# Kernel tuning notes

Measured on AMD Instinct MI355X. Metric: run time of the kernel, lower is better.

## Reference

```python
import jax, jax.numpy as jnp
import numpy as np

N = 50000          # num nodes
E = 800000         # num edges (avg degree 16)
IN_C, HID_C, OUT_C = 128, 128, 64
LPA_ITER = 5


def setup_inputs() -> dict:
    key = jax.random.key(0)
    ks = jax.random.split(key, 8)
    x = jax.random.normal(ks[0], (N, IN_C), dtype=jnp.float32)
    soft_labels = jax.random.uniform(ks[1], (N, OUT_C), dtype=jnp.float32)
    edge_index = jax.random.randint(ks[2], (2, E), 0, N, dtype=jnp.int64)
    # learnable edge weights: abs() in the original, so keep them positive
    edge_attr = jax.random.uniform(ks[3], (E,), dtype=jnp.float32, minval=0.1, maxval=1.0)
    # GCNConv params (lin weight + bias)
    w1 = jax.random.normal(ks[4], (IN_C, HID_C), dtype=jnp.float32) / np.sqrt(IN_C)
    b1 = jnp.zeros((HID_C,), dtype=jnp.float32)
    w2 = jax.random.normal(ks[5], (HID_C, OUT_C), dtype=jnp.float32) / np.sqrt(HID_C)
    b2 = jnp.zeros((OUT_C,), dtype=jnp.float32)
    return {"x": x, "soft_labels": soft_labels, "edge_attr": edge_attr,
            "w1": w1, "b1": b1, "w2": w2, "b2": b2, "edge_index": edge_index}


def reference(x, soft_labels, edge_attr, w1, b1, w2, b2, edge_index):
    row, col = edge_index[0], edge_index[1]
    n = x.shape[0]
    # row-normalize the weighted sparse adjacency: A_n = D^{-1} A
    deg = jax.ops.segment_sum(edge_attr, row, num_segments=n)  # [N]
    deg_inv = jnp.where(deg == 0, 0.0, 1.0 / deg)              # inf -> 0
    val = deg_inv[row] * edge_attr                              # [E]

    def spmm(v):  # A_n @ v,  v: [N, F]
        return jax.ops.segment_sum(val[:, None] * v[col], row, num_segments=n)

    # eval mode: dropout(p=0.5, training=False) is identity
    h = jax.nn.relu(spmm(x @ w1) + b1)        # GCNConv 1 (normalize=False)
    logits = spmm(h @ w2) + b2                # GCNConv 2
    x_out = jax.nn.sigmoid(logits)

    labels = soft_labels
    for _ in range(LPA_ITER):                 # label propagation
        labels = spmm(labels)
    labels = jax.nn.sigmoid(labels)
    return (x_out, labels)
```

## Files before the change

### kernel.cpp

```cpp
#include <hip/hip_runtime.h>
#include <cstdint>
#include <cstddef>


#define WS_ALIGN(x) (((x) + 255) & ~((size_t)255))

typedef __attribute__((ext_vector_type(8))) short short8;
typedef __attribute__((ext_vector_type(4))) float floatx4;

__device__ __forceinline__ unsigned short f2bf(float f) {
    unsigned u = __float_as_uint(f);
    u += 0x7fffu + ((u >> 16) & 1u);
    return (unsigned short)(u >> 16);
}
__device__ __forceinline__ float bf2f(unsigned short h) {
    return __uint_as_float(((unsigned)h) << 16);
}
__device__ __forceinline__ float sigmoidf(float x) {
    return 1.f / (1.f + __expf(-x));
}

static const int NBLK = 256;
#define MAXNB 256

__launch_bounds__(256)
__global__ void binA_count(const int* __restrict__ row, int* __restrict__ bucket_count,
                           int* __restrict__ bases, int E, int chunk, int NB)
{
    __shared__ int hist[MAXNB];
    const int t = threadIdx.x;
    const int blk = blockIdx.x;
    if (t < NB) hist[t] = 0;
    __syncthreads();
    const int s = blk * chunk;
    const int e = min(E, s + chunk);
    for (int i = s + t; i < e; i += 256)
        atomicAdd(&hist[row[i] >> 8], 1);
    __syncthreads();
    if (t < NB)
        bases[blk * NB + t] = atomicAdd(&bucket_count[t], hist[t]);
}

__launch_bounds__(256)
__global__ void bin_scan(const int* __restrict__ bucket_count, int* __restrict__ bucket_start,
                         int NB)
{
    __shared__ int s[256];
    const int t = threadIdx.x;
    int v = (t < NB) ? bucket_count[t] : 0;
    s[t] = v;
    __syncthreads();
    for (int off = 1; off < 256; off <<= 1) {
        int u = (t >= off) ? s[t - off] : 0;
        __syncthreads();
        s[t] += u;
        __syncthreads();
    }
    int excl = s[t] - v;
    if (t <= NB) bucket_start[t] = excl;
}

__launch_bounds__(256)
__global__ void binA_scatter(const int* __restrict__ row, const int* __restrict__ colv,
                             const float* __restrict__ ea,
                             const int* __restrict__ bucket_start, const int* __restrict__ bases,
                             int2* __restrict__ bk, int E, int chunk, int NB)
{
    __shared__ int cur[MAXNB];
    const int t = threadIdx.x;
    const int blk = blockIdx.x;
    if (t < NB) cur[t] = bucket_start[t] + bases[blk * NB + t];
    __syncthreads();
    const int s = blk * chunk;
    const int e = min(E, s + chunk);
    for (int i = s + t; i < e; i += 256) {
        int r = row[i];
        int bin = r >> 8;
        int pos = atomicAdd(&cur[bin], 1);
        bk[pos] = make_int2(((r & 255) << 16) | colv[i], __float_as_int(ea[i]));
    }
}

__launch_bounds__(256)
__global__ void binB(const int2* __restrict__ bk, const int* __restrict__ bucket_start,
                     int* __restrict__ rowptr, int2* __restrict__ edges, int N)
{
    __shared__ int cnt[256];
    __shared__ float deg[256];
    __shared__ float inv[256];
    __shared__ int excl_s[256];
    __shared__ int cur[256];
    __shared__ int scantmp[256];
    const int b = blockIdx.x;
    const int t = threadIdx.x;
    const int s = bucket_start[b];
    const int e = bucket_start[b + 1];
    cnt[t] = 0;
    deg[t] = 0.f;
    __syncthreads();
    for (int i = s + t; i < e; i += 256) {
        int2 v = bk[i];
        int rl = ((unsigned)v.x) >> 16;
        atomicAdd(&cnt[rl], 1);
        atomicAdd(&deg[rl], __int_as_float(v.y));
    }
    __syncthreads();
    const int myc = cnt[t];
    scantmp[t] = myc;
    __syncthreads();
    for (int off = 1; off < 256; off <<= 1) {
        int u = (t >= off) ? scantmp[t - off] : 0;
        __syncthreads();
        scantmp[t] += u;
        __syncthreads();
    }
    const int excl = scantmp[t] - myc;
    excl_s[t] = excl;
    float d = deg[t];
    inv[t] = (d > 0.f) ? 1.f / d : 0.f;
    cur[t] = 0;
    const int gr = b * 256 + t;
    if (gr <= N) rowptr[gr] = s + excl;
    __syncthreads();
    for (int i = s + t; i < e; i += 256) {
        int2 v = bk[i];
        int rl = ((unsigned)v.x) >> 16;
        int c = v.x & 0xffff;
        int p = s + excl_s[rl] + atomicAdd(&cur[rl], 1);
        edges[p] = make_int2(c, __float_as_int(__int_as_float(v.y) * inv[rl]));
    }
}

__global__ void f32_to_bf16_kernel(const float* __restrict__ in, unsigned short* __restrict__ out,
                                   int n2)
{
    int i = blockIdx.x * 256 + threadIdx.x;
    if (i < n2) {
        float2 v = ((const float2*)in)[i];
        unsigned p = (unsigned)f2bf(v.x) | ((unsigned)f2bf(v.y) << 16);
        ((unsigned*)out)[i] = p;
    }
}

template<int COLS>
__global__ void pack_w_kernel(const float* __restrict__ W, unsigned short* __restrict__ Wp)
{
    const int total = (COLS / 16) * 4 * 64;
    int idx = blockIdx.x * 256 + threadIdx.x;
    if (idx >= total) return;
    const int l = idx & 63;
    const int t = (idx >> 6) & 3;
    const int ct = idx >> 8;
    const int kbase = t * 32 + (l >> 4) * 8;
    const int col = ct * 16 + (l & 15);
    unsigned short v[8];
#pragma unroll
    for (int j = 0; j < 8; ++j)
        v[j] = f2bf(W[(size_t)(kbase + j) * COLS + col]);
    uint4 o;
    o.x = (unsigned)v[0] | ((unsigned)v[1] << 16);
    o.y = (unsigned)v[2] | ((unsigned)v[3] << 16);
    o.z = (unsigned)v[4] | ((unsigned)v[5] << 16);
    o.w = (unsigned)v[6] | ((unsigned)v[7] << 16);
    *(uint4*)(Wp + (size_t)idx * 8) = o;
}

template<int COLS>
__launch_bounds__(256)
__global__ void gemm_mfma_f32a(const float* __restrict__ A,
                               const unsigned short* __restrict__ Wp,
                               unsigned short* __restrict__ C, int M)
{
    const int wave = threadIdx.x >> 6;
    const int lane = threadIdx.x & 63;
    const int row0 = blockIdx.x * 64 + wave * 16;
    const int m = lane & 15;
    const int q = lane >> 4;

    const int arow = row0 + m;
    const bool avalid = arow < M;
    short8 a[4];
#pragma unroll
    for (int t = 0; t < 4; ++t) {
        if (avalid) {
            float4 f0 = *(const float4*)(A + (size_t)arow * 128 + t * 32 + q * 8);
            float4 f1 = *(const float4*)(A + (size_t)arow * 128 + t * 32 + q * 8 + 4);
            a[t][0] = (short)f2bf(f0.x); a[t][1] = (short)f2bf(f0.y);
            a[t][2] = (short)f2bf(f0.z); a[t][3] = (short)f2bf(f0.w);
            a[t][4] = (short)f2bf(f1.x); a[t][5] = (short)f2bf(f1.y);
            a[t][6] = (short)f2bf(f1.z); a[t][7] = (short)f2bf(f1.w);
        } else {
            a[t] = (short8)0;
        }
    }

#pragma unroll
    for (int ct = 0; ct < COLS / 16; ++ct) {
        floatx4 acc = {0.f, 0.f, 0.f, 0.f};
#pragma unroll
        for (int t = 0; t < 4; ++t) {
            short8 b = *(const short8*)(Wp + (size_t)((ct * 4 + t) * 64 + lane) * 8);
            acc = __builtin_amdgcn_mfma_f32_16x16x32_bf16(a[t], b, acc, 0, 0, 0);
        }
        const int col = ct * 16 + m;
#pragma unroll
        for (int r = 0; r < 4; ++r) {
            int orow = row0 + q * 4 + r;
            if (orow < M)
                C[(size_t)orow * COLS + col] = f2bf(acc[r]);
        }
    }
}

template<int COLS>
__launch_bounds__(256)
__global__ void gemm_mfma(const unsigned short* __restrict__ A,
                          const unsigned short* __restrict__ Wp,
                          unsigned short* __restrict__ C, int M)
{
    const int wave = threadIdx.x >> 6;
    const int lane = threadIdx.x & 63;
    const int row0 = blockIdx.x * 64 + wave * 16;
    const int m = lane & 15;
    const int q = lane >> 4;

    const int arow = row0 + m;
    const bool avalid = arow < M;
    short8 a[4];
#pragma unroll
    for (int t = 0; t < 4; ++t) {
        if (avalid)
            a[t] = *(const short8*)(A + (size_t)arow * 128 + t * 32 + q * 8);
        else
            a[t] = (short8)0;
    }

#pragma unroll
    for (int ct = 0; ct < COLS / 16; ++ct) {
        floatx4 acc = {0.f, 0.f, 0.f, 0.f};
#pragma unroll
        for (int t = 0; t < 4; ++t) {
            short8 b = *(const short8*)(Wp + (size_t)((ct * 4 + t) * 64 + lane) * 8);
            acc = __builtin_amdgcn_mfma_f32_16x16x32_bf16(a[t], b, acc, 0, 0, 0);
        }
        const int col = ct * 16 + m;
#pragma unroll
        for (int r = 0; r < 4; ++r) {
            int orow = row0 + q * 4 + r;
            if (orow < M)
                C[(size_t)orow * COLS + col] = f2bf(acc[r]);
        }
    }
}

__launch_bounds__(256)
__global__ void spmm_f128_f64(const int* __restrict__ rowptr, const int2* __restrict__ edges,
                              const unsigned* __restrict__ srcA,
                              const unsigned short* __restrict__ srcB,
                              const float* __restrict__ bias,
                              unsigned* __restrict__ outA,
                              unsigned short* __restrict__ outB,
                              int n)
{
    const int row = blockIdx.x * 4 + (threadIdx.x >> 6);
    const int lane = threadIdx.x & 63;
    if (row >= n) return;
    const int s = rowptr[row];
    const int e = rowptr[row + 1];

    float ax[8], ay[8], ab[8];
#pragma unroll
    for (int j = 0; j < 8; ++j) { ax[j] = 0.f; ay[j] = 0.f; ab[j] = 0.f; }
    int i = s;
    for (; i + 8 <= e; i += 8) {
        int2 ed[8];
        unsigned ua[8];
        unsigned short ub[8];
#pragma unroll
        for (int j = 0; j < 8; ++j) ed[j] = edges[i + j];
#pragma unroll
        for (int j = 0; j < 8; ++j) ua[j] = srcA[(size_t)ed[j].x * 64 + lane];
#pragma unroll
        for (int j = 0; j < 8; ++j) ub[j] = srcB[(size_t)ed[j].x * 64 + lane];
#pragma unroll
        for (int j = 0; j < 8; ++j) {
            float w = __int_as_float(ed[j].y);
            ax[j] = fmaf(w, __uint_as_float(ua[j] << 16), ax[j]);
            ay[j] = fmaf(w, __uint_as_float(ua[j] & 0xffff0000u), ay[j]);
            ab[j] = fmaf(w, bf2f(ub[j]), ab[j]);
        }
    }
    for (; i < e; ++i) {
        int2 e0 = edges[i];
        unsigned ua = srcA[(size_t)e0.x * 64 + lane];
        unsigned short ub = srcB[(size_t)e0.x * 64 + lane];
        float w = __int_as_float(e0.y);
        ax[0] = fmaf(w, __uint_as_float(ua << 16), ax[0]);
        ay[0] = fmaf(w, __uint_as_float(ua & 0xffff0000u), ay[0]);
        ab[0] = fmaf(w, bf2f(ub), ab[0]);
    }
    float vx = ((ax[0] + ax[1]) + (ax[2] + ax[3])) + ((ax[4] + ax[5]) + (ax[6] + ax[7]));
    float vy = ((ay[0] + ay[1]) + (ay[2] + ay[3])) + ((ay[4] + ay[5]) + (ay[6] + ay[7]));
    float vb = ((ab[0] + ab[1]) + (ab[2] + ab[3])) + ((ab[4] + ab[5]) + (ab[6] + ab[7]));
    float2 b = *(const float2*)(bias + lane * 2);
    vx = fmaxf(vx + b.x, 0.f);
    vy = fmaxf(vy + b.y, 0.f);
    outA[(size_t)row * 64 + lane] = (unsigned)f2bf(vx) | ((unsigned)f2bf(vy) << 16);
    outB[(size_t)row * 64 + lane] = f2bf(vb);
}

__launch_bounds__(256)
__global__ void spmm_f64_f64(const int* __restrict__ rowptr, const int2* __restrict__ edges,
                             const unsigned short* __restrict__ srcA,
                             const unsigned short* __restrict__ srcB,
                             const float* __restrict__ bias,
                             float* __restrict__ outA,
                             unsigned short* __restrict__ outB,
                             int n)
{
    const int row = blockIdx.x * 4 + (threadIdx.x >> 6);
    const int lane = threadIdx.x & 63;
    if (row >= n) return;
    const int s = rowptr[row];
    const int e = rowptr[row + 1];

    float aa[8], ab[8];
#pragma unroll
    for (int j = 0; j < 8; ++j) { aa[j] = 0.f; ab[j] = 0.f; }
    int i = s;
    for (; i + 8 <= e; i += 8) {
        int2 ed[8];
        unsigned short ua[8], ub[8];
#pragma unroll
        for (int j = 0; j < 8; ++j) ed[j] = edges[i + j];
#pragma unroll
        for (int j = 0; j < 8; ++j) ua[j] = srcA[(size_t)ed[j].x * 64 + lane];
#pragma unroll
        for (int j = 0; j < 8; ++j) ub[j] = srcB[(size_t)ed[j].x * 64 + lane];
#pragma unroll
        for (int j = 0; j < 8; ++j) {
            float w = __int_as_float(ed[j].y);
            aa[j] = fmaf(w, bf2f(ua[j]), aa[j]);
            ab[j] = fmaf(w, bf2f(ub[j]), ab[j]);
        }
    }
    for (; i < e; ++i) {
        int2 e0 = edges[i];
        float w = __int_as_float(e0.y);
        aa[0] = fmaf(w, bf2f(srcA[(size_t)e0.x * 64 + lane]), aa[0]);
        ab[0] = fmaf(w, bf2f(srcB[(size_t)e0.x * 64 + lane]), ab[0]);
    }
    float va = ((aa[0] + aa[1]) + (aa[2] + aa[3])) + ((aa[4] + aa[5]) + (aa[6] + aa[7]));
    float vb = ((ab[0] + ab[1]) + (ab[2] + ab[3])) + ((ab[4] + ab[5]) + (ab[6] + ab[7]));
    outA[(size_t)row * 64 + lane] = sigmoidf(va + bias[lane]);
    outB[(size_t)row * 64 + lane] = f2bf(vb);
}

template<int ACT, bool OUT_BF16>
__launch_bounds__(256)
__global__ void spmm64_kernel(const int* __restrict__ rowptr, const int2* __restrict__ edges,
                              const unsigned short* __restrict__ src,
                              void* __restrict__ out, int n)
{
    const int row = blockIdx.x * 4 + (threadIdx.x >> 6);
    const int lane = threadIdx.x & 63;
    if (row >= n) return;
    const int s = rowptr[row];
    const int e = rowptr[row + 1];

    float a[8];
#pragma unroll
    for (int j = 0; j < 8; ++j) a[j] = 0.f;
    int i = s;
    for (; i + 8 <= e; i += 8) {
        int2 ed[8];
        float sv[8];
#pragma unroll
        for (int j = 0; j < 8; ++j) ed[j] = edges[i + j];
#pragma unroll
        for (int j = 0; j < 8; ++j) sv[j] = bf2f(src[(size_t)ed[j].x * 64 + lane]);
#pragma unroll
        for (int j = 0; j < 8; ++j) a[j] = fmaf(__int_as_float(ed[j].y), sv[j], a[j]);
    }
    for (; i < e; ++i) {
        int2 e0 = edges[i];
        a[0] = fmaf(__int_as_float(e0.y), bf2f(src[(size_t)e0.x * 64 + lane]), a[0]);
    }
    float v = ((a[0] + a[1]) + (a[2] + a[3])) + ((a[4] + a[5]) + (a[6] + a[7]));
    if (ACT == 3) v = sigmoidf(v);
    if (OUT_BF16)
        ((unsigned short*)out)[(size_t)row * 64 + lane] = f2bf(v);
    else
        ((float*)out)[(size_t)row * 64 + lane] = v;
}

extern "C" void kernel_launch(void* const* d_in, const int* in_sizes, int n_in,
                              void* d_out, int out_size, void* d_ws, size_t ws_size,
                              hipStream_t stream)
{
    const float* x    = (const float*)d_in[0];
    const float* soft = (const float*)d_in[1];
    const float* ea   = (const float*)d_in[2];
    const float* w1   = (const float*)d_in[3];
    const float* b1   = (const float*)d_in[4];
    const float* w2   = (const float*)d_in[5];
    const float* b2   = (const float*)d_in[6];
    const int*   eidx = (const int*)d_in[7];

    const int N = in_sizes[0] / 128;
    const int E = in_sizes[2];
    const int* row  = eidx;
    const int* colv = eidx + E;
    const int NB = (N + 255) / 256;
    const int chunk = (E + NBLK - 1) / NBLK;

    uint8_t* ws = (uint8_t*)d_ws;
    size_t off = 0;
    auto alloc = [&](size_t bytes) -> void* {
        void* p = ws + off;
        off += WS_ALIGN(bytes);
        return p;
    };
    int*  bucket_count = (int*) alloc((size_t)NB * 4);
    int*  bucket_start = (int*) alloc(((size_t)NB + 1) * 4);
    int*  bases        = (int*) alloc((size_t)NBLK * NB * 4);
    int*  rowptr       = (int*) alloc(((size_t)N + 1) * 4);
    int2* bk           = (int2*)alloc((size_t)E * 8);
    int2* edges        = (int2*)alloc((size_t)E * 8);
    unsigned short* w1p     = (unsigned short*)alloc((size_t)128 * 128 * 2);
    unsigned short* w2p     = (unsigned short*)alloc((size_t)128 * 64 * 2);
    unsigned short* xw1b    = (unsigned short*)alloc((size_t)N * 128 * 2);
    unsigned short* hb      = (unsigned short*)alloc((size_t)N * 128 * 2);
    unsigned short* logitsb = (unsigned short*)alloc((size_t)N * 64 * 2);
    unsigned short* softb   = (unsigned short*)alloc((size_t)N * 64 * 2);
    unsigned short* labA    = (unsigned short*)alloc((size_t)N * 64 * 2);
    unsigned short* labB    = (unsigned short*)alloc((size_t)N * 64 * 2);

    float* out0 = (float*)d_out;
    float* out1 = out0 + (size_t)N * 64;

    hipMemsetAsync(bucket_count, 0, (size_t)NB * 4, stream);

    binA_count<<<NBLK, 256, 0, stream>>>(row, bucket_count, bases, E, chunk, NB);
    bin_scan<<<1, 256, 0, stream>>>(bucket_count, bucket_start, NB);
    binA_scatter<<<NBLK, 256, 0, stream>>>(row, colv, ea, bucket_start, bases, bk, E, chunk, NB);
    binB<<<NB, 256, 0, stream>>>(bk, bucket_start, rowptr, edges, N);

    const int ns2 = (N * 64) / 2;
    f32_to_bf16_kernel<<<(ns2 + 255) / 256, 256, 0, stream>>>(soft, softb, ns2);
    pack_w_kernel<128><<<8, 256, 0, stream>>>(w1, w1p);
    pack_w_kernel<64><<<4, 256, 0, stream>>>(w2, w2p);

    const int gGemm = (N + 63) / 64;
    const int gSp   = (N + 3) / 4;

    gemm_mfma_f32a<128><<<gGemm, 256, 0, stream>>>(x, w1p, xw1b, N);

    spmm_f128_f64<<<gSp, 256, 0, stream>>>(rowptr, edges, (const unsigned*)xw1b, softb,
                                           b1, (unsigned*)hb, labA, N);

    gemm_mfma<64><<<gGemm, 256, 0, stream>>>(hb, w2p, logitsb, N);

    spmm_f64_f64<<<gSp, 256, 0, stream>>>(rowptr, edges, logitsb, labA, b2, out0, labB, N);

    spmm64_kernel<0, true ><<<gSp, 256, 0, stream>>>(rowptr, edges, labB, labA, N);
    spmm64_kernel<0, true ><<<gSp, 256, 0, stream>>>(rowptr, edges, labA, labB, N);
    spmm64_kernel<3, false><<<gSp, 256, 0, stream>>>(rowptr, edges, labB, out1, N);
}
```

Measured before the change: 361.9 us.

## Split wavefront into two half-waves gathering wider vectors per edge in SpMM kernels

Each 64-lane wavefront now processes two edges at once, with each 32-lane half loading wider packed bf16 vectors (uint2 or unsigned) per feature slice. The halves are combined with a cross-lane shuffle before the write. Edge records are read with nontemporal loads. The aim is fewer, wider gather transactions per row and fewer serial edge iterations. The cost is an extra shuffle reduction and idle half-waves on odd tail edges.

```diff
diff --git a/kernel.cpp b/kernel.cpp
--- a/kernel.cpp
+++ b/kernel.cpp
@@ -13,11 +13,23 @@
     u += 0x7fffu + ((u >> 16) & 1u);
     return (unsigned short)(u >> 16);
 }
+__device__ __forceinline__ float bf_lo(unsigned u) { return __uint_as_float(u << 16); }
+__device__ __forceinline__ float bf_hi(unsigned u) { return __uint_as_float(u & 0xffff0000u); }
 __device__ __forceinline__ float bf2f(unsigned short h) {
     return __uint_as_float(((unsigned)h) << 16);
 }
+__device__ __forceinline__ unsigned pack_bf2(float a, float b) {
+    return (unsigned)f2bf(a) | ((unsigned)f2bf(b) << 16);
+}
 __device__ __forceinline__ float sigmoidf(float x) {
     return 1.f / (1.f + __expf(-x));
+}
+__device__ __forceinline__ int2 ld_nt_int2(const int2* p) {
+    long long v = __builtin_nontemporal_load((const long long*)p);
+    int2 r;
+    r.x = (int)(unsigned)(v & 0xffffffffLL);
+    r.y = (int)(v >> 32);
+    return r;
 }
 
 static const int NBLK = 256;
@@ -137,8 +149,7 @@
     int i = blockIdx.x * 256 + threadIdx.x;
     if (i < n2) {
         float2 v = ((const float2*)in)[i];
-        unsigned p = (unsigned)f2bf(v.x) | ((unsigned)f2bf(v.y) << 16);
-        ((unsigned*)out)[i] = p;
+        ((unsigned*)out)[i] = pack_bf2(v.x, v.y);
     }
 }
 
@@ -254,144 +265,228 @@
 }
 
 __launch_bounds__(256)
-__global__ void spmm_f128_f64(const int* __restrict__ rowptr, const int2* __restrict__ edges,
-                              const unsigned* __restrict__ srcA,
-                              const unsigned short* __restrict__ srcB,
-                              const float* __restrict__ bias,
-                              unsigned* __restrict__ outA,
-                              unsigned short* __restrict__ outB,
-                              int n)
+__global__ void fused1_pair(const int* __restrict__ rowptr, const int2* __restrict__ edges,
+                            const uint2* __restrict__ srcA,
+                            const unsigned* __restrict__ srcB,
+                            const float* __restrict__ bias,
+                            uint2* __restrict__ outA,
+                            unsigned* __restrict__ outB,
+                            int n)
 {
     const int row = blockIdx.x * 4 + (threadIdx.x >> 6);
     const int lane = threadIdx.x & 63;
+    const int f = lane & 31;
+    const int half = lane >> 5;
     if (row >= n) return;
     const int s = rowptr[row];
     const int e = rowptr[row + 1];
 
-    float ax[8], ay[8], ab[8];
-#pragma unroll
-    for (int j = 0; j < 8; ++j) { ax[j] = 0.f; ay[j] = 0.f; ab[j] = 0.f; }
+    float a0[4], a1[4], b0[2], b1[2];
+#pragma unroll
+    for (int j = 0; j < 4; ++j) { a0[j] = 0.f; a1[j] = 0.f; }
+    b0[0] = b0[1] = b1[0] = b1[1] = 0.f;
+
     int i = s;
     for (; i + 8 <= e; i += 8) {
-        int2 ed[8];
-        unsigned ua[8];
-        unsigned short ub[8];
-#pragma unroll
-        for (int j = 0; j < 8; ++j) ed[j] = edges[i + j];
-#pragma unroll
-        for (int j = 0; j < 8; ++j) ua[j] = srcA[(size_t)ed[j].x * 64 + lane];
-#pragma unroll
-        for (int j = 0; j < 8; ++j) ub[j] = srcB[(size_t)ed[j].x * 64 + lane];
-#pragma unroll
-        for (int j = 0; j < 8; ++j) {
+        int2 ed[4]; uint2 ua[4]; unsigned ub[4];
+#pragma unroll
+        for (int j = 0; j < 4; ++j) ed[j] = ld_nt_int2(&edges[i + 2 * j + half]);
+#pragma unroll
+        for (int j = 0; j < 4; ++j) ua[j] = srcA[(size_t)ed[j].x * 32 + f];
+#pragma unroll
+        for (int j = 0; j < 4; ++j) ub[j] = srcB[(size_t)ed[j].x * 32 + f];
+#pragma unroll
+        for (int j = 0; j < 4; ++j) {
             float w = __int_as_float(ed[j].y);
-            ax[j] = fmaf(w, __uint_as_float(ua[j] << 16), ax[j]);
-            ay[j] = fmaf(w, __uint_as_float(ua[j] & 0xffff0000u), ay[j]);
-            ab[j] = fmaf(w, bf2f(ub[j]), ab[j]);
-        }
-    }
-    for (; i < e; ++i) {
-        int2 e0 = edges[i];
-        unsigned ua = srcA[(size_t)e0.x * 64 + lane];
-        unsigned short ub = srcB[(size_t)e0.x * 64 + lane];
-        float w = __int_as_float(e0.y);
-        ax[0] = fmaf(w, __uint_as_float(ua << 16), ax[0]);
-        ay[0] = fmaf(w, __uint_as_float(ua & 0xffff0000u), ay[0]);
-        ab[0] = fmaf(w, bf2f(ub), ab[0]);
-    }
-    float vx = ((ax[0] + ax[1]) + (ax[2] + ax[3])) + ((ax[4] + ax[5]) + (ax[6] + ax[7]));
-    float vy = ((ay[0] + ay[1]) + (ay[2] + ay[3])) + ((ay[4] + ay[5]) + (ay[6] + ay[7]));
-    float vb = ((ab[0] + ab[1]) + (ab[2] + ab[3])) + ((ab[4] + ab[5]) + (ab[6] + ab[7]));
-    float2 b = *(const float2*)(bias + lane * 2);
-    vx = fmaxf(vx + b.x, 0.f);
-    vy = fmaxf(vy + b.y, 0.f);
-    outA[(size_t)row * 64 + lane] = (unsigned)f2bf(vx) | ((unsigned)f2bf(vy) << 16);
-    outB[(size_t)row * 64 + lane] = f2bf(vb);
-}
-
-__launch_bounds__(256)
-__global__ void spmm_f64_f64(const int* __restrict__ rowptr, const int2* __restrict__ edges,
-                             const unsigned short* __restrict__ srcA,
-                             const unsigned short* __restrict__ srcB,
-                             const float* __restrict__ bias,
-                             float* __restrict__ outA,
-                             unsigned short* __restrict__ outB,
-                             int n)
+            float* A = (j & 1) ? a1 : a0;
+            float* B = (j & 1) ? b1 : b0;
+            A[0] = fmaf(w, bf_lo(ua[j].x), A[0]);
+            A[1] = fmaf(w, bf_hi(ua[j].x), A[1]);
+            A[2] = fmaf(w, bf_lo(ua[j].y), A[2]);
+            A[3] = fmaf(w, bf_hi(ua[j].y), A[3]);
+            B[0] = fmaf(w, bf_lo(ub[j]), B[0]);
+            B[1] = fmaf(w, bf_hi(ub[j]), B[1]);
+        }
+    }
+    for (; i + 2 <= e; i += 2) {
+        int2 ed = ld_nt_int2(&edges[i + half]);
+        float w = __int_as_float(ed.y);
+        uint2 ua = srcA[(size_t)ed.x * 32 + f];
+        unsigned ub = srcB[(size_t)ed.x * 32 + f];
+        a0[0] = fmaf(w, bf_lo(ua.x), a0[0]);
+        a0[1] = fmaf(w, bf_hi(ua.x), a0[1]);
+        a0[2] = fmaf(w, bf_lo(ua.y), a0[2]);
+        a0[3] = fmaf(w, bf_hi(ua.y), a0[3]);
+        b0[0] = fmaf(w, bf_lo(ub), b0[0]);
+        b0[1] = fmaf(w, bf_hi(ub), b0[1]);
+    }
+    if (i < e && half == 0) {
+        int2 ed = ld_nt_int2(&edges[i]);
+        float w = __int_as_float(ed.y);
+        uint2 ua = srcA[(size_t)ed.x * 32 + f];
+        unsigned ub = srcB[(size_t)ed.x * 32 + f];
+        a1[0] = fmaf(w, bf_lo(ua.x), a1[0]);
+        a1[1] = fmaf(w, bf_hi(ua.x), a1[1]);
+        a1[2] = fmaf(w, bf_lo(ua.y), a1[2]);
+        a1[3] = fmaf(w, bf_hi(ua.y), a1[3]);
+        b1[0] = fmaf(w, bf_lo(ub), b1[0]);
+        b1[1] = fmaf(w, bf_hi(ub), b1[1]);
+    }
+    float A0 = a0[0] + a1[0], A1 = a0[1] + a1[1];
+    float A2 = a0[2] + a1[2], A3 = a0[3] + a1[3];
+    float B0 = b0[0] + b1[0], B1 = b0[1] + b1[1];
+    A0 += __shfl_down(A0, 32); A1 += __shfl_down(A1, 32);
+    A2 += __shfl_down(A2, 32); A3 += __shfl_down(A3, 32);
+    B0 += __shfl_down(B0, 32); B1 += __shfl_down(B1, 32);
+    if (half == 0) {
+        float4 bb = *(const float4*)(bias + 4 * f);
+        A0 = fmaxf(A0 + bb.x, 0.f);
+        A1 = fmaxf(A1 + bb.y, 0.f);
+        A2 = fmaxf(A2 + bb.z, 0.f);
+        A3 = fmaxf(A3 + bb.w, 0.f);
+        uint2 o;
+        o.x = pack_bf2(A0, A1);
+        o.y = pack_bf2(A2, A3);
+        outA[(size_t)row * 32 + f] = o;
+        outB[(size_t)row * 32 + f] = pack_bf2(B0, B1);
+    }
+}
+
+__launch_bounds__(256)
+__global__ void fused2_pair(const int* __restrict__ rowptr, const int2* __restrict__ edges,
+                            const unsigned* __restrict__ srcA,
+                            const unsigned* __restrict__ srcB,
+                            const float* __restrict__ bias,
+                            float* __restrict__ outA,
+                            unsigned* __restrict__ outB,
+                            int n)
 {
     const int row = blockIdx.x * 4 + (threadIdx.x >> 6);
     const int lane = threadIdx.x & 63;
+    const int f = lane & 31;
+    const int half = lane >> 5;
     if (row >= n) return;
     const int s = rowptr[row];
     const int e = rowptr[row + 1];
 
-    float aa[8], ab[8];
-#pragma unroll
-    for (int j = 0; j < 8; ++j) { aa[j] = 0.f; ab[j] = 0.f; }
+    float a0[2], a1[2], b0[2], b1[2];
+    a0[0] = a0[1] = a1[0] = a1[1] = 0.f;
+    b0[0] = b0[1] = b1[0] = b1[1] = 0.f;
+
     int i = s;
     for (; i + 8 <= e; i += 8) {
-        int2 ed[8];
-        unsigned short ua[8], ub[8];
-#pragma unroll
-        for (int j = 0; j < 8; ++j) ed[j] = edges[i + j];
-#pragma unroll
-        for (int j = 0; j < 8; ++j) ua[j] = srcA[(size_t)ed[j].x * 64 + lane];
-#pragma unroll
-        for (int j = 0; j < 8; ++j) ub[j] = srcB[(size_t)ed[j].x * 64 + lane];
-#pragma unroll
-        for (int j = 0; j < 8; ++j) {
+        int2 ed[4]; unsigned ua[4], ub[4];
+#pragma unroll
+        for (int j = 0; j < 4; ++j) ed[j] = ld_nt_int2(&edges[i + 2 * j + half]);
+#pragma unroll
+        for (int j = 0; j < 4; ++j) ua[j] = srcA[(size_t)ed[j].x * 32 + f];
+#pragma unroll
+        for (int j = 0; j < 4; ++j) ub[j] = srcB[(size_t)ed[j].x * 32 + f];
+#pragma unroll
+        for (int j = 0; j < 4; ++j) {
             float w = __int_as_float(ed[j].y);
-            aa[j] = fmaf(w, bf2f(ua[j]), aa[j]);
-            ab[j] = fmaf(w, bf2f(ub[j]), ab[j]);
-        }
-    }
-    for (; i < e; ++i) {
-        int2 e0 = edges[i];
-        float w = __int_as_float(e0.y);
-        aa[0] = fmaf(w, bf2f(srcA[(size_t)e0.x * 64 + lane]), aa[0]);
-        ab[0] = fmaf(w, bf2f(srcB[(size_t)e0.x * 64 + lane]), ab[0]);
-    }
-    float va = ((aa[0] + aa[1]) + (aa[2] + aa[3])) + ((aa[4] + aa[5]) + (aa[6] + aa[7]));
-    float vb = ((ab[0] + ab[1]) + (ab[2] + ab[3])) + ((ab[4] + ab[5]) + (ab[6] + ab[7]));
-    outA[(size_t)row * 64 + lane] = sigmoidf(va + bias[lane]);
-    outB[(size_t)row * 64 + lane] = f2bf(vb);
-}
-
-template<int ACT, bool OUT_BF16>
-__launch_bounds__(256)
-__global__ void spmm64_kernel(const int* __restrict__ rowptr, const int2* __restrict__ edges,
-                              const unsigned short* __restrict__ src,
-                              void* __restrict__ out, int n)
+            float* A = (j & 1) ? a1 : a0;
+            float* B = (j & 1) ? b1 : b0;
+            A[0] = fmaf(w, bf_lo(ua[j]), A[0]);
+            A[1] = fmaf(w, bf_hi(ua[j]), A[1]);
+            B[0] = fmaf(w, bf_lo(ub[j]), B[0]);
+            B[1] = fmaf(w, bf_hi(ub[j]), B[1]);
+        }
+    }
+    for (; i + 2 <= e; i += 2) {
+        int2 ed = ld_nt_int2(&edges[i + half]);
+        float w = __int_as_float(ed.y);
+        unsigned ua = srcA[(size_t)ed.x * 32 + f];
+        unsigned ub = srcB[(size_t)ed.x * 32 + f];
+        a0[0] = fmaf(w, bf_lo(ua), a0[0]);
+        a0[1] = fmaf(w, bf_hi(ua), a0[1]);
+        b0[0] = fmaf(w, bf_lo(ub), b0[0]);
+        b0[1] = fmaf(w, bf_hi(ub), b0[1]);
+    }
+    if (i < e && half == 0) {
+        int2 ed = ld_nt_int2(&edges[i]);
+        float w = __int_as_float(ed.y);
+        unsigned ua = srcA[(size_t)ed.x * 32 + f];
+        unsigned ub = srcB[(size_t)ed.x * 32 + f];
+        a1[0] = fmaf(w, bf_lo(ua), a1[0]);
+        a1[1] = fmaf(w, bf_hi(ua), a1[1]);
+        b1[0] = fmaf(w, bf_lo(ub), b1[0]);
+        b1[1] = fmaf(w, bf_hi(ub), b1[1]);
+    }
+    float A0 = a0[0] + a1[0], A1 = a0[1] + a1[1];
+    float B0 = b0[0] + b1[0], B1 = b0[1] + b1[1];
+    A0 += __shfl_down(A0, 32); A1 += __shfl_down(A1, 32);
+    B0 += __shfl_down(B0, 32); B1 += __shfl_down(B1, 32);
+    if (half == 0) {
+        float2 bb = *(const float2*)(bias + 2 * f);
+        float2 o;
+        o.x = sigmoidf(A0 + bb.x);
+        o.y = sigmoidf(A1 + bb.y);
+        *(float2*)(outA + (size_t)row * 64 + 2 * f) = o;
+        outB[(size_t)row * 32 + f] = pack_bf2(B0, B1);
+    }
+}
+
+template<int ACT>
+__launch_bounds__(256)
+__global__ void spmm64_pair(const int* __restrict__ rowptr, const int2* __restrict__ edges,
+                            const unsigned* __restrict__ src,
+                            void* __restrict__ out, int n)
 {
     const int row = blockIdx.x * 4 + (threadIdx.x >> 6);
     const int lane = threadIdx.x & 63;
+    const int f = lane & 31;
+    const int half = lane >> 5;
     if (row >= n) return;
     const int s = rowptr[row];
     const int e = rowptr[row + 1];
 
-    float a[8];
-#pragma unroll
-    for (int j = 0; j < 8; ++j) a[j] = 0.f;
+    float a[4][2];
+#pragma unroll
+    for (int j = 0; j < 4; ++j) { a[j][0] = 0.f; a[j][1] = 0.f; }
+
     int i = s;
     for (; i + 8 <= e; i += 8) {
-        int2 ed[8];
-        float sv[8];
-#pragma unroll
-        for (int j = 0; j < 8; ++j) ed[j] = edges[i + j];
-#pragma unroll
-        for (int j = 0; j < 8; ++j) sv[j] = bf2f(src[(size_t)ed[j].x * 64 + lane]);
-#pragma unroll
-        for (int j = 0; j < 8; ++j) a[j] = fmaf(__int_as_float(ed[j].y), sv[j], a[j]);
-    }
-    for (; i < e; ++i) {
-        int2 e0 = edges[i];
-        a[0] = fmaf(__int_as_float(e0.y), bf2f(src[(size_t)e0.x * 64 + lane]), a[0]);
-    }
-    float v = ((a[0] + a[1]) + (a[2] + a[3])) + ((a[4] + a[5]) + (a[6] + a[7]));
-    if (ACT == 3) v = sigmoidf(v);
-    if (OUT_BF16)
-        ((unsigned short*)out)[(size_t)row * 64 + lane] = f2bf(v);
-    else
-        ((float*)out)[(size_t)row * 64 + lane] = v;
+        int2 ed[4]; unsigned u[4];
+#pragma unroll
+        for (int j = 0; j < 4; ++j) ed[j] = ld_nt_int2(&edges[i + 2 * j + half]);
+#pragma unroll
+        for (int j = 0; j < 4; ++j) u[j] = src[(size_t)ed[j].x * 32 + f];
+#pragma unroll
+        for (int j = 0; j < 4; ++j) {
+            float w = __int_as_float(ed[j].y);
+            a[j][0] = fmaf(w, bf_lo(u[j]), a[j][0]);
+            a[j][1] = fmaf(w, bf_hi(u[j]), a[j][1]);
+        }
+    }
+    for (; i + 2 <= e; i += 2) {
+        int2 ed = ld_nt_int2(&edges[i + half]);
+        float w = __int_as_float(ed.y);
+        unsigned u = src[(size_t)ed.x * 32 + f];
+        a[0][0] = fmaf(w, bf_lo(u), a[0][0]);
+        a[0][1] = fmaf(w, bf_hi(u), a[0][1]);
+    }
+    if (i < e && half == 0) {
+        int2 ed = ld_nt_int2(&edges[i]);
+        float w = __int_as_float(ed.y);
+        unsigned u = src[(size_t)ed.x * 32 + f];
+        a[1][0] = fmaf(w, bf_lo(u), a[1][0]);
+        a[1][1] = fmaf(w, bf_hi(u), a[1][1]);
+    }
+    float v0 = (a[0][0] + a[1][0]) + (a[2][0] + a[3][0]);
+    float v1 = (a[0][1] + a[1][1]) + (a[2][1] + a[3][1]);
+    v0 += __shfl_down(v0, 32);
+    v1 += __shfl_down(v1, 32);
+    if (half == 0) {
+        if (ACT == 0) {
+            ((unsigned*)out)[(size_t)row * 32 + f] = pack_bf2(v0, v1);
+        } else {
+            float2 o;
+            o.x = sigmoidf(v0);
+            o.y = sigmoidf(v1);
+            *(float2*)((float*)out + (size_t)row * 64 + 2 * f) = o;
+        }
+    }
 }
 
 extern "C" void kernel_launch(void* const* d_in, const int* in_sizes, int n_in,
@@ -456,14 +551,17 @@
 
     gemm_mfma_f32a<128><<<gGemm, 256, 0, stream>>>(x, w1p, xw1b, N);
 
-    spmm_f128_f64<<<gSp, 256, 0, stream>>>(rowptr, edges, (const unsigned*)xw1b, softb,
-                                           b1, (unsigned*)hb, labA, N);
+    fused1_pair<<<gSp, 256, 0, stream>>>(rowptr, edges, (const uint2*)xw1b,
+                                         (const unsigned*)softb, b1,
+                                         (uint2*)hb, (unsigned*)labA, N);
 
     gemm_mfma<64><<<gGemm, 256, 0, stream>>>(hb, w2p, logitsb, N);
 
-    spmm_f64_f64<<<gSp, 256, 0, stream>>>(rowptr, edges, logitsb, labA, b2, out0, labB, N);
-
-    spmm64_kernel<0, true ><<<gSp, 256, 0, stream>>>(rowptr, edges, labB, labA, N);
-    spmm64_kernel<0, true ><<<gSp, 256, 0, stream>>>(rowptr, edges, labA, labB, N);
-    spmm64_kernel<3, false><<<gSp, 256, 0, stream>>>(rowptr, edges, labB, out1, N);
-}
+    fused2_pair<<<gSp, 256, 0, stream>>>(rowptr, edges, (const unsigned*)logitsb,
+                                         (const unsigned*)labA, b2,
+                                         out0, (unsigned*)labB, N);
+
+    spmm64_pair<0><<<gSp, 256, 0, stream>>>(rowptr, edges, (const unsigned*)labB, labA, N);
+    spmm64_pair<0><<<gSp, 256, 0, stream>>>(rowptr, edges, (const unsigned*)labA, labB, N);
+    spmm64_pair<3><<<gSp, 256, 0, stream>>>(rowptr, edges, (const unsigned*)labB, out1, N);
+}
```

New measurement: 317.8 us. 1.14x faster.
